# Kernel tuning notes

Hardware: AMD Instinct MI355X
Metric: run time of the kernel (lower is better)

Reference implementation:

```python
import jax, jax.numpy as jnp
import numpy as np

B, N_CGS, N_ATOMS, KNN, K, DEPTH = 16, 256, 1024, 32, 128, 3
CUTOFF = 10.0


def _init_params(key):
    ks = jax.random.split(key, 12)
    s = 1.0 / np.sqrt(K)
    p = {}
    # stacked per-depth settransform weights: Linear stored as [in, out] (y = x @ W + b)
    p['mlp_W1'] = jax.random.normal(ks[0], (DEPTH, K, K), jnp.float32) * s
    p['mlp_b1'] = jnp.zeros((DEPTH, K), jnp.float32)
    p['mlp_W2'] = jax.random.normal(ks[1], (DEPTH, K, K), jnp.float32) * s
    p['mlp_b2'] = jnp.zeros((DEPTH, K), jnp.float32)
    p['upd_W1'] = jax.random.normal(ks[2], (DEPTH, K, K), jnp.float32) * s
    p['upd_b1'] = jnp.zeros((DEPTH, K), jnp.float32)
    p['upd_W2'] = jax.random.normal(ks[3], (DEPTH, K, K), jnp.float32) * s
    p['upd_b2'] = jnp.zeros((DEPTH, K), jnp.float32)
    p['dec_W1'] = jax.random.normal(ks[4], (K, K), jnp.float32) * s
    p['dec_b1'] = jnp.zeros((K,), jnp.float32)
    p['dec_W2'] = jax.random.normal(ks[5], (K, N_ATOMS), jnp.float32) * s
    p['dec_b2'] = jnp.zeros((N_ATOMS,), jnp.float32)
    return p


def setup_inputs() -> dict:
    key = jax.random.key(0)
    ks = jax.random.split(key, 6)
    inp = {
        'soft_assign': jax.random.uniform(ks[0], (B, N_ATOMS, N_CGS), jnp.float32),
        'xyz': jax.random.normal(ks[1], (B, N_ATOMS, 3), jnp.float32),
        'cg_xyz': jax.random.normal(ks[2], (B, N_CGS, 3), jnp.float32),
        'assign_norm': jax.random.uniform(ks[3], (B, N_ATOMS, N_CGS), jnp.float32),
        'assign_idx': jax.random.randint(ks[4], (N_ATOMS,), 0, N_CGS, jnp.int32),
    }
    inp.update(_init_params(ks[5]))
    return inp


def _forward(cg_xyz, assign_norm, assign_idx,
             mlp_W1, mlp_b1, mlp_W2, mlp_b2,
             upd_W1, upd_b1, upd_W2, upd_b2,
             dec_W1, dec_b1, dec_W2, dec_b2):
    act = jax.nn.relu
    # Pairwise CG distance + ascending sort (as in source). The source then
    # zeroes sorted values beyond rank knn and uses value.nonzero()[:, 1:] as
    # neighbor pairs, i.e. it indexes by SORT RANK (ranks 1..knn), not by the
    # sorted index tensor knbrs. For generic (distinct) coordinates this is
    # exactly: neighbor j in {1..knn} for every center i. We replicate that.
    dist_vec = cg_xyz[:, None, 1:KNN + 1, :] - cg_xyz[:, :, None, :]  # [B, n_cgs, knn, 3]
    dist_vec = dist_vec.reshape(B, N_CGS * KNN, 3)
    dist = jnp.sqrt(jnp.sum(dist_vec ** 2, axis=-1)).reshape(B, N_CGS, KNN, 1)

    # GaussianSmearing(0, cutoff, feature_dim)
    offset = jnp.linspace(0.0, CUTOFF, K)  # [K]
    coeff = -0.5 / (offset[1] - offset[0]) ** 2
    out = jnp.exp(coeff * (dist - offset) ** 2)  # [B, n_cgs, knn, K]

    # settransform layers (loop over small fixed depth)
    for d in range(DEPTH):
        upd = act(out @ mlp_W1[d] + mlp_b1[d]) @ mlp_W2[d] + mlp_b2[d]
        cg_contract = jnp.mean(upd, axis=-2, keepdims=True)  # mean over knn axis
        h = upd + cg_contract
        out = act(h @ upd_W1[d] + upd_b1[d]) @ upd_W2[d] + upd_b2[d]

    # decode K -> n_atoms
    coeffs = (act(out @ dec_W1 + dec_b1) @ dec_W2 + dec_b2)
    coeffs = coeffs.reshape(B, N_CGS * KNN, N_ATOMS)

    dx_recon = jnp.einsum('bio,bin->bon', coeffs, dist_vec)      # [B, n_atoms, 3]
    cg_offset = jnp.einsum('bin,bij->bjn', dx_recon, assign_norm)  # [B, n_cgs, 3]
    cg_offset_lift = cg_offset[:, assign_idx, :]                  # [B, n_atoms, 3]
    xyz_recon = cg_xyz[:, assign_idx, :] - cg_offset_lift + dx_recon
    return xyz_recon


def reference(soft_assign, xyz, cg_xyz, assign_norm, assign_idx,
              mlp_W1, mlp_b1, mlp_W2, mlp_b2,
              upd_W1, upd_b1, upd_W2, upd_b2,
              dec_W1, dec_b1, dec_W2, dec_b2):
    xyz_recon = _forward(cg_xyz, assign_norm, assign_idx,
                         mlp_W1, mlp_b1, mlp_W2, mlp_b2,
                         upd_W1, upd_b1, upd_W2, upd_b2,
                         dec_W1, dec_b1, dec_W2, dec_b2)
    return (soft_assign, xyz, xyz_recon)
```

## Files before the change

kernel.cpp:

```cpp
#include <hip/hip_runtime.h>

#define BATCH   16
#define NCGS    256
#define NATOMS  1024
#define KNN     32
#define KF      128

typedef __attribute__((ext_vector_type(8))) short bf16x8;
typedef __attribute__((ext_vector_type(4))) float f32x4;

#define NFRAG (13*8*4)

__global__ __launch_bounds__(256)
void prep_kernel(const float* __restrict__ mlp_W1, const float* __restrict__ mlp_W2,
                 const float* __restrict__ upd_W1, const float* __restrict__ upd_W2,
                 const float* __restrict__ dec_W1, uint* __restrict__ Wswz)
{
    int t = blockIdx.x * 256 + threadIdx.x;
    if (t >= 13*8*4*64) return;
    int lane = t & 63;
    int kc   = (t >> 6) & 3;
    int ft   = (t >> 8) & 7;
    int s    = t >> 11;

    const float* W;
    if (s < 12) {
        int d = s >> 2, ph = s & 3;
        if      (ph == 0) W = mlp_W1 + d*KF*KF;
        else if (ph == 1) W = mlp_W2 + d*KF*KF;
        else if (ph == 2) W = upd_W1 + d*KF*KF;
        else              W = upd_W2 + d*KF*KF;
    } else W = dec_W1;

    int f  = ft*16 + (lane & 15);
    int kb = kc*32 + (lane >> 4)*8;

    uint hi[4], lo[4];
    #pragma unroll
    for (int w = 0; w < 4; ++w) {
        float v0 = W[(kb + 2*w    )*KF + f];
        float v1 = W[(kb + 2*w + 1)*KF + f];
        uint b0 = __float_as_uint(v0), b1 = __float_as_uint(v1);
        hi[w] = (b0 >> 16) | (b1 & 0xffff0000u);
        float l0 = v0 - __uint_as_float(b0 & 0xffff0000u);
        float l1 = v1 - __uint_as_float(b1 & 0xffff0000u);
        lo[w] = (__float_as_uint(l0) >> 16) | (__float_as_uint(l1) & 0xffff0000u);
    }
    int fi = (s*8 + ft)*4 + kc;
    uint* ph_ = Wswz + (size_t)((fi*2 + 0)*64 + lane)*4;
    uint* pl_ = Wswz + (size_t)((fi*2 + 1)*64 + lane)*4;
    #pragma unroll
    for (int w = 0; w < 4; ++w) { ph_[w] = hi[w]; pl_[w] = lo[w]; }
}

__global__ __launch_bounds__(256, 2)
void mlp_kernel(const float* __restrict__ cg_xyz, const bf16x8* __restrict__ Wf,
                const float* __restrict__ mlp_b1, const float* __restrict__ mlp_b2,
                const float* __restrict__ upd_b1, const float* __restrict__ upd_b2,
                const float* __restrict__ dec_b1, float* __restrict__ G)
{
    __shared__ __align__(16) short Fs[2][KF*KF];
    __shared__ float dvec[128*3];

    const int tid = threadIdx.x;
    const int wv  = tid >> 6;
    const int l   = tid & 63;
    const int b   = blockIdx.x >> 6;
    const int cg0 = (blockIdx.x & 63) * 4;
    const int cg  = cg0 + wv;

    char* hB = (char*)&Fs[0][0];
    char* lB = (char*)&Fs[1][0];

    const float* cgb = cg_xyz + (size_t)b * NCGS * 3;
    const int rl = l & 31;
    const int nb = 1 + rl;
    float dxv = cgb[nb*3+0] - cgb[cg*3+0];
    float dyv = cgb[nb*3+1] - cgb[cg*3+1];
    float dzv = cgb[nb*3+2] - cgb[cg*3+2];
    float dist = sqrtf(dxv*dxv + dyv*dyv + dzv*dzv);
    if (l < 32) {
        int r = wv*32 + rl;
        dvec[r*3+0] = dxv; dvec[r*3+1] = dyv; dvec[r*3+2] = dzv;
    }

    {
        const float STEP  = 10.0f / 127.0f;
        const float COEFF = -0.5f / (STEP * STEP);
        int r  = wv*32 + rl;
        int kh = (l >> 5) * 64;
        uint rb = (uint)r * 256;
        uint sw = (uint)(r & 7) << 4;
        #pragma unroll 8
        for (int j = 0; j < 32; ++j) {
            int k = kh + 2*j;
            float t0 = dist - (float)k * STEP;
            float t1 = dist - (float)(k+1) * STEP;
            float e0 = expf(COEFF * t0 * t0);
            float e1 = expf(COEFF * t1 * t1);
            uint b0 = __float_as_uint(e0), b1 = __float_as_uint(e1);
            uint hw = (b0 >> 16) | (b1 & 0xffff0000u);
            float l0 = e0 - __uint_as_float(b0 & 0xffff0000u);
            float l1 = e1 - __uint_as_float(b1 & 0xffff0000u);
            uint lw = (__float_as_uint(l0) >> 16) | (__float_as_uint(l1) & 0xffff0000u);
            uint off = rb + (((uint)(2*k)) ^ sw);
            *(uint*)(hB + off) = hw;
            *(uint*)(lB + off) = lw;
        }
    }

    for (int s = 0; s < 13; ++s) {
        const float* bias; int md;
        if (s < 12) {
            int d = s >> 2, ph = s & 3;
            if      (ph == 0) { bias = mlp_b1 + d*KF; md = 0; }
            else if (ph == 1) { bias = mlp_b2 + d*KF; md = 1; }
            else if (ph == 2) { bias = upd_b1 + d*KF; md = 0; }
            else              { bias = upd_b2 + d*KF; md = 2; }
        } else { bias = dec_b1; md = 0; }

        bf16x8 bf[2][4][2];
        #pragma unroll
        for (int rt = 0; rt < 2; ++rt) {
            int r = wv*32 + rt*16 + (l & 15);
            uint rb = (uint)r * 256;
            uint sw = (uint)(r & 7) << 4;
            #pragma unroll
            for (int kc = 0; kc < 4; ++kc) {
                uint cb = (uint)(kc*64 + ((l >> 4) << 4));
                uint off = rb + (cb ^ sw);
                bf[rt][kc][0] = *(const bf16x8*)(hB + off);
                bf[rt][kc][1] = *(const bf16x8*)(lB + off);
            }
        }

        f32x4 acc[8][2];
        #pragma unroll
        for (int ft = 0; ft < 8; ++ft)
            #pragma unroll
            for (int rt = 0; rt < 2; ++rt)
                acc[ft][rt] = (f32x4){0.f, 0.f, 0.f, 0.f};

        #pragma unroll
        for (int kc = 0; kc < 4; ++kc) {
            #pragma unroll
            for (int ft = 0; ft < 8; ++ft) {
                int fi = (s*8 + ft)*4 + kc;
                bf16x8 whi = Wf[(fi*2 + 0)*64 + l];
                bf16x8 wlo = Wf[(fi*2 + 1)*64 + l];
                #pragma unroll
                for (int rt = 0; rt < 2; ++rt) {
                    acc[ft][rt] = __builtin_amdgcn_mfma_f32_16x16x32_bf16(whi, bf[rt][kc][0], acc[ft][rt], 0, 0, 0);
                    acc[ft][rt] = __builtin_amdgcn_mfma_f32_16x16x32_bf16(whi, bf[rt][kc][1], acc[ft][rt], 0, 0, 0);
                    acc[ft][rt] = __builtin_amdgcn_mfma_f32_16x16x32_bf16(wlo, bf[rt][kc][0], acc[ft][rt], 0, 0, 0);
                }
            }
        }

        #pragma unroll
        for (int ft = 0; ft < 8; ++ft) {
            float4 bv = *(const float4*)(bias + ft*16 + ((l >> 4) << 2));
            #pragma unroll
            for (int rt = 0; rt < 2; ++rt) {
                acc[ft][rt][0] += bv.x; acc[ft][rt][1] += bv.y;
                acc[ft][rt][2] += bv.z; acc[ft][rt][3] += bv.w;
            }
        }
        if (md == 0) {
            #pragma unroll
            for (int ft = 0; ft < 8; ++ft)
                #pragma unroll
                for (int rt = 0; rt < 2; ++rt)
                    #pragma unroll
                    for (int q = 0; q < 4; ++q)
                        acc[ft][rt][q] = fmaxf(acc[ft][rt][q], 0.f);
        } else if (md == 1) {
            #pragma unroll
            for (int ft = 0; ft < 8; ++ft)
                #pragma unroll
                for (int q = 0; q < 4; ++q) {
                    float sm = acc[ft][0][q] + acc[ft][1][q];
                    sm += __shfl_xor(sm, 1);
                    sm += __shfl_xor(sm, 2);
                    sm += __shfl_xor(sm, 4);
                    sm += __shfl_xor(sm, 8);
                    float mn = sm * (1.0f / 32.0f);
                    acc[ft][0][q] += mn;
                    acc[ft][1][q] += mn;
                }
        }
        #pragma unroll
        for (int ft = 0; ft < 8; ++ft) {
            #pragma unroll
            for (int rt = 0; rt < 2; ++rt) {
                int r = wv*32 + rt*16 + (l & 15);
                uint sw  = (uint)(r & 7) << 4;
                uint off = (uint)r*256 + (((uint)(ft*32 + ((l >> 4) << 3))) ^ sw);
                uint b0 = __float_as_uint(acc[ft][rt][0]);
                uint b1 = __float_as_uint(acc[ft][rt][1]);
                uint b2 = __float_as_uint(acc[ft][rt][2]);
                uint b3 = __float_as_uint(acc[ft][rt][3]);
                uint2 hw, lw;
                hw.x = (b0 >> 16) | (b1 & 0xffff0000u);
                hw.y = (b2 >> 16) | (b3 & 0xffff0000u);
                float l0 = acc[ft][rt][0] - __uint_as_float(b0 & 0xffff0000u);
                float l1 = acc[ft][rt][1] - __uint_as_float(b1 & 0xffff0000u);
                float l2 = acc[ft][rt][2] - __uint_as_float(b2 & 0xffff0000u);
                float l3 = acc[ft][rt][3] - __uint_as_float(b3 & 0xffff0000u);
                lw.x = (__float_as_uint(l0) >> 16) | (__float_as_uint(l1) & 0xffff0000u);
                lw.y = (__float_as_uint(l2) >> 16) | (__float_as_uint(l3) & 0xffff0000u);
                *(uint2*)(hB + off) = hw;
                *(uint2*)(lB + off) = lw;
            }
        }
    }
    __syncthreads();

    {
        int k  = tid & 127;
        int rh = tid >> 7;
        float g0 = 0.f, g1 = 0.f, g2 = 0.f;
        #pragma unroll 4
        for (int rr = 0; rr < 64; ++rr) {
            int r = rh*64 + rr;
            uint off = (uint)r*256 + (((uint)(2*k)) ^ ((uint)(r & 7) << 4));
            uint hv = *(unsigned short*)(hB + off);
            uint lv = *(unsigned short*)(lB + off);
            float v = __uint_as_float(hv << 16) + __uint_as_float(lv << 16);
            g0 = fmaf(v, dvec[r*3+0], g0);
            g1 = fmaf(v, dvec[r*3+1], g1);
            g2 = fmaf(v, dvec[r*3+2], g2);
        }
        float* Gb = G + ((size_t)b * KF + k) * 3;
        atomicAdd(Gb+0, g0); atomicAdd(Gb+1, g1); atomicAdd(Gb+2, g2);
    }
}

__global__ __launch_bounds__(256)
void dx_kernel(const float* __restrict__ cg_xyz, const float* __restrict__ dec_W2,
               const float* __restrict__ dec_b2, const float* __restrict__ G,
               float* __restrict__ dxr)
{
    __shared__ float Gl[KF * 3];
    __shared__ float red[256 * 3];
    const int tid = threadIdx.x;
    const int b   = blockIdx.x >> 2;
    const int og  = blockIdx.x & 3;

    if (tid < 192) {
        Gl[tid]       = G[(size_t)b*KF*3 + tid];
        Gl[tid + 192] = G[(size_t)b*KF*3 + tid + 192];
    }
    const float* cgb = cg_xyz + (size_t)b * NCGS * 3;
    float w = ((tid >= 1 && tid <= 32) ? 256.f : 0.f) - 32.f;
    red[tid]       = w * cgb[tid*3+0];
    red[256 + tid] = w * cgb[tid*3+1];
    red[512 + tid] = w * cgb[tid*3+2];
    __syncthreads();
    for (int s2 = 128; s2 > 0; s2 >>= 1) {
        if (tid < s2) {
            red[tid]       += red[tid + s2];
            red[256 + tid] += red[256 + tid + s2];
            red[512 + tid] += red[512 + tid + s2];
        }
        __syncthreads();
    }
    const float S0 = red[0], S1 = red[256], S2 = red[512];

    const int o = og * 256 + tid;
    const float bq = dec_b2[o];
    float a0 = bq * S0, a1 = bq * S1, a2 = bq * S2;
    #pragma unroll 4
    for (int k = 0; k < KF; ++k) {
        float wvv = dec_W2[k * NATOMS + o];
        a0 = fmaf(wvv, Gl[k*3+0], a0);
        a1 = fmaf(wvv, Gl[k*3+1], a1);
        a2 = fmaf(wvv, Gl[k*3+2], a2);
    }
    float* dp = dxr + ((size_t)b * NATOMS + o) * 3;
    dp[0] = a0; dp[1] = a1; dp[2] = a2;
}

__global__ __launch_bounds__(256)
void cgo_kernel(const float* __restrict__ assign_norm, const float* __restrict__ dxr,
                float* __restrict__ cgo)
{
    __shared__ float dxl[64 * 3];
    const int tid = threadIdx.x;
    const int b   = blockIdx.x >> 4;
    const int a0  = (blockIdx.x & 15) * 64;
    if (tid < 192) dxl[tid] = dxr[((size_t)b * NATOMS + a0) * 3 + tid];
    __syncthreads();
    float c0 = 0.f, c1 = 0.f, c2 = 0.f;
    const float* an = assign_norm + ((size_t)b * NATOMS + a0) * NCGS + tid;
    #pragma unroll 4
    for (int a = 0; a < 64; ++a) {
        float v = an[(size_t)a * NCGS];
        c0 = fmaf(v, dxl[a*3+0], c0);
        c1 = fmaf(v, dxl[a*3+1], c1);
        c2 = fmaf(v, dxl[a*3+2], c2);
    }
    float* cp = cgo + ((size_t)b * NCGS + tid) * 3;
    atomicAdd(cp+0, c0); atomicAdd(cp+1, c1); atomicAdd(cp+2, c2);
}

__global__ __launch_bounds__(256)
void recon_kernel(const float* __restrict__ cg_xyz, const float* __restrict__ cgo,
                  const float* __restrict__ dxr, const int* __restrict__ assign_idx,
                  float* __restrict__ out)
{
    int i = blockIdx.x * 256 + threadIdx.x;
    int b   = i / (NATOMS * 3);
    int rem = i - b * (NATOMS * 3);
    int a   = rem / 3;
    int n   = rem - a * 3;
    int ia  = assign_idx[a];
    float v = cg_xyz[((size_t)b*NCGS + ia)*3 + n]
            - cgo[((size_t)b*NCGS + ia)*3 + n]
            + dxr[((size_t)b*NATOMS + a)*3 + n];
    out[i] = v;
}

extern "C" void kernel_launch(void* const* d_in, const int* in_sizes, int n_in,
                              void* d_out, int out_size, void* d_ws, size_t ws_size,
                              hipStream_t stream)
{
    const float* soft_assign = (const float*)d_in[0];
    const float* xyz         = (const float*)d_in[1];
    const float* cg_xyz      = (const float*)d_in[2];
    const float* assign_norm = (const float*)d_in[3];
    const int*   assign_idx  = (const int*)  d_in[4];
    const float* mlp_W1 = (const float*)d_in[5];
    const float* mlp_b1 = (const float*)d_in[6];
    const float* mlp_W2 = (const float*)d_in[7];
    const float* mlp_b2 = (const float*)d_in[8];
    const float* upd_W1 = (const float*)d_in[9];
    const float* upd_b1 = (const float*)d_in[10];
    const float* upd_W2 = (const float*)d_in[11];
    const float* upd_b2 = (const float*)d_in[12];
    const float* dec_W1 = (const float*)d_in[13];
    const float* dec_b1 = (const float*)d_in[14];
    const float* dec_W2 = (const float*)d_in[15];
    const float* dec_b2 = (const float*)d_in[16];

    float* out = (float*)d_out;

    uint*  Wswz = (uint*)d_ws;
    float* G    = (float*)d_ws + NFRAG*2*64*4;
    float* cgo  = G + BATCH * KF * 3;
    float* dxr  = cgo + BATCH * NCGS * 3;

    hipMemcpyAsync(out, soft_assign, (size_t)BATCH*NATOMS*NCGS*sizeof(float),
                   hipMemcpyDeviceToDevice, stream);
    hipMemcpyAsync(out + (size_t)BATCH*NATOMS*NCGS, xyz,
                   (size_t)BATCH*NATOMS*3*sizeof(float),
                   hipMemcpyDeviceToDevice, stream);
    hipMemsetAsync(G, 0, (size_t)(BATCH*KF*3 + BATCH*NCGS*3)*sizeof(float), stream);

    prep_kernel<<<104, 256, 0, stream>>>(mlp_W1, mlp_W2, upd_W1, upd_W2, dec_W1, Wswz);
    mlp_kernel<<<BATCH*64, 256, 0, stream>>>(cg_xyz, (const bf16x8*)Wswz,
        mlp_b1, mlp_b2, upd_b1, upd_b2, dec_b1, G);
    dx_kernel<<<BATCH*4, 256, 0, stream>>>(cg_xyz, dec_W2, dec_b2, G, dxr);
    cgo_kernel<<<BATCH*16, 256, 0, stream>>>(assign_norm, dxr, cgo);
    recon_kernel<<<(BATCH*NATOMS*3)/256, 256, 0, stream>>>(
        cg_xyz, cgo, dxr, assign_idx,
        out + (size_t)BATCH*NATOMS*NCGS + (size_t)BATCH*NATOMS*3);
}
```

Measured before the change: 341.7 us.

## Keep MLP activations in registers and permute weight K-order to skip LDS

The 13-stage MLP chain now keeps the hi/lo bf16 activation fragments in registers between stages instead of round-tripping them through shared memory. The weight prep permutes the K ordering for stages after the first so that MFMA accumulator outputs map directly onto the next stage's B-operand layout. The final G reduction is done with lane shuffles and scattered over 8 partial slices to spread atomic contention, and dx_kernel sums those slices. This removes LDS traffic and barriers and may raise occupancy, at the cost of higher register pressure and more atomics per block.

```diff
diff --git a/kernel.cpp b/kernel.cpp
--- a/kernel.cpp
+++ b/kernel.cpp
@@ -5,11 +5,14 @@
 #define NATOMS  1024
 #define KNN     32
 #define KF      128
+#define NSLICE  8
 
 typedef __attribute__((ext_vector_type(8))) short bf16x8;
 typedef __attribute__((ext_vector_type(4))) float f32x4;
 
 #define NFRAG (13*8*4)
+
+union U16B { bf16x8 v; uint u[4]; };
 
 __global__ __launch_bounds__(256)
 void prep_kernel(const float* __restrict__ mlp_W1, const float* __restrict__ mlp_W2,
@@ -32,14 +35,17 @@
         else              W = upd_W2 + d*KF*KF;
     } else W = dec_W1;
 
-    int f  = ft*16 + (lane & 15);
-    int kb = kc*32 + (lane >> 4)*8;
+    int f = ft*16 + (lane & 15);
+    int g = lane >> 4;
 
     uint hi[4], lo[4];
     #pragma unroll
     for (int w = 0; w < 4; ++w) {
-        float v0 = W[(kb + 2*w    )*KF + f];
-        float v1 = W[(kb + 2*w + 1)*KF + f];
+        int k0;
+        if (s == 0) k0 = kc*32 + g*8 + 2*w;
+        else        k0 = kc*16 + (w>>1)*64 + g*4 + 2*(w&1);
+        float v0 = W[(size_t)k0*KF + f];
+        float v1 = W[(size_t)(k0+1)*KF + f];
         uint b0 = __float_as_uint(v0), b1 = __float_as_uint(v1);
         hi[w] = (b0 >> 16) | (b1 & 0xffff0000u);
         float l0 = v0 - __uint_as_float(b0 & 0xffff0000u);
@@ -57,58 +63,50 @@
 void mlp_kernel(const float* __restrict__ cg_xyz, const bf16x8* __restrict__ Wf,
                 const float* __restrict__ mlp_b1, const float* __restrict__ mlp_b2,
                 const float* __restrict__ upd_b1, const float* __restrict__ upd_b2,
-                const float* __restrict__ dec_b1, float* __restrict__ G)
-{
-    __shared__ __align__(16) short Fs[2][KF*KF];
-    __shared__ float dvec[128*3];
-
+                const float* __restrict__ dec_b1, float* __restrict__ Gp)
+{
     const int tid = threadIdx.x;
     const int wv  = tid >> 6;
     const int l   = tid & 63;
+    const int g   = l >> 4;
+    const int e0  = l & 15;
     const int b   = blockIdx.x >> 6;
-    const int cg0 = (blockIdx.x & 63) * 4;
-    const int cg  = cg0 + wv;
-
-    char* hB = (char*)&Fs[0][0];
-    char* lB = (char*)&Fs[1][0];
+    const int cg  = (blockIdx.x & 63) * 4 + wv;
 
     const float* cgb = cg_xyz + (size_t)b * NCGS * 3;
-    const int rl = l & 31;
-    const int nb = 1 + rl;
-    float dxv = cgb[nb*3+0] - cgb[cg*3+0];
-    float dyv = cgb[nb*3+1] - cgb[cg*3+1];
-    float dzv = cgb[nb*3+2] - cgb[cg*3+2];
-    float dist = sqrtf(dxv*dxv + dyv*dyv + dzv*dzv);
-    if (l < 32) {
-        int r = wv*32 + rl;
-        dvec[r*3+0] = dxv; dvec[r*3+1] = dyv; dvec[r*3+2] = dzv;
-    }
-
-    {
-        const float STEP  = 10.0f / 127.0f;
-        const float COEFF = -0.5f / (STEP * STEP);
-        int r  = wv*32 + rl;
-        int kh = (l >> 5) * 64;
-        uint rb = (uint)r * 256;
-        uint sw = (uint)(r & 7) << 4;
-        #pragma unroll 8
-        for (int j = 0; j < 32; ++j) {
-            int k = kh + 2*j;
-            float t0 = dist - (float)k * STEP;
-            float t1 = dist - (float)(k+1) * STEP;
-            float e0 = expf(COEFF * t0 * t0);
-            float e1 = expf(COEFF * t1 * t1);
-            uint b0 = __float_as_uint(e0), b1 = __float_as_uint(e1);
-            uint hw = (b0 >> 16) | (b1 & 0xffff0000u);
-            float l0 = e0 - __uint_as_float(b0 & 0xffff0000u);
-            float l1 = e1 - __uint_as_float(b1 & 0xffff0000u);
-            uint lw = (__float_as_uint(l0) >> 16) | (__float_as_uint(l1) & 0xffff0000u);
-            uint off = rb + (((uint)(2*k)) ^ sw);
-            *(uint*)(hB + off) = hw;
-            *(uint*)(lB + off) = lw;
-        }
-    }
-
+    const float cx = cgb[cg*3+0], cy = cgb[cg*3+1], cz = cgb[cg*3+2];
+    const float d0x = cgb[(1+e0)*3+0]-cx,  d0y = cgb[(1+e0)*3+1]-cy,  d0z = cgb[(1+e0)*3+2]-cz;
+    const float d1x = cgb[(17+e0)*3+0]-cx, d1y = cgb[(17+e0)*3+1]-cy, d1z = cgb[(17+e0)*3+2]-cz;
+    const float dist0 = sqrtf(d0x*d0x + d0y*d0y + d0z*d0z);
+    const float dist1 = sqrtf(d1x*d1x + d1y*d1y + d1z*d1z);
+
+    const float STEP  = 10.0f / 127.0f;
+    const float COEFF = -0.5f / (STEP * STEP);
+    bf16x8 bh[2][4], bl[2][4];
+    #pragma unroll
+    for (int rt = 0; rt < 2; ++rt) {
+        float dd = rt ? dist1 : dist0;
+        #pragma unroll
+        for (int kc = 0; kc < 4; ++kc) {
+            U16B H, L;
+            #pragma unroll
+            for (int w = 0; w < 4; ++w) {
+                int k0 = kc*32 + g*8 + 2*w;
+                float t0 = dd - (float)k0 * STEP;
+                float t1 = dd - (float)(k0+1) * STEP;
+                float e0f = expf(COEFF * t0 * t0);
+                float e1f = expf(COEFF * t1 * t1);
+                uint b0 = __float_as_uint(e0f), b1 = __float_as_uint(e1f);
+                H.u[w] = (b0 >> 16) | (b1 & 0xffff0000u);
+                float l0 = e0f - __uint_as_float(b0 & 0xffff0000u);
+                float l1 = e1f - __uint_as_float(b1 & 0xffff0000u);
+                L.u[w] = (__float_as_uint(l0) >> 16) | (__float_as_uint(l1) & 0xffff0000u);
+            }
+            bh[rt][kc] = H.v; bl[rt][kc] = L.v;
+        }
+    }
+
+    f32x4 acc[8][2];
     for (int s = 0; s < 13; ++s) {
         const float* bias; int md;
         if (s < 12) {
@@ -119,22 +117,6 @@
             else              { bias = upd_b2 + d*KF; md = 2; }
         } else { bias = dec_b1; md = 0; }
 
-        bf16x8 bf[2][4][2];
-        #pragma unroll
-        for (int rt = 0; rt < 2; ++rt) {
-            int r = wv*32 + rt*16 + (l & 15);
-            uint rb = (uint)r * 256;
-            uint sw = (uint)(r & 7) << 4;
-            #pragma unroll
-            for (int kc = 0; kc < 4; ++kc) {
-                uint cb = (uint)(kc*64 + ((l >> 4) << 4));
-                uint off = rb + (cb ^ sw);
-                bf[rt][kc][0] = *(const bf16x8*)(hB + off);
-                bf[rt][kc][1] = *(const bf16x8*)(lB + off);
-            }
-        }
-
-        f32x4 acc[8][2];
         #pragma unroll
         for (int ft = 0; ft < 8; ++ft)
             #pragma unroll
@@ -150,16 +132,16 @@
                 bf16x8 wlo = Wf[(fi*2 + 1)*64 + l];
                 #pragma unroll
                 for (int rt = 0; rt < 2; ++rt) {
-                    acc[ft][rt] = __builtin_amdgcn_mfma_f32_16x16x32_bf16(whi, bf[rt][kc][0], acc[ft][rt], 0, 0, 0);
-                    acc[ft][rt] = __builtin_amdgcn_mfma_f32_16x16x32_bf16(whi, bf[rt][kc][1], acc[ft][rt], 0, 0, 0);
-                    acc[ft][rt] = __builtin_amdgcn_mfma_f32_16x16x32_bf16(wlo, bf[rt][kc][0], acc[ft][rt], 0, 0, 0);
+                    acc[ft][rt] = __builtin_amdgcn_mfma_f32_16x16x32_bf16(whi, bh[rt][kc], acc[ft][rt], 0, 0, 0);
+                    acc[ft][rt] = __builtin_amdgcn_mfma_f32_16x16x32_bf16(whi, bl[rt][kc], acc[ft][rt], 0, 0, 0);
+                    acc[ft][rt] = __builtin_amdgcn_mfma_f32_16x16x32_bf16(wlo, bh[rt][kc], acc[ft][rt], 0, 0, 0);
                 }
             }
         }
 
         #pragma unroll
         for (int ft = 0; ft < 8; ++ft) {
-            float4 bv = *(const float4*)(bias + ft*16 + ((l >> 4) << 2));
+            float4 bv = *(const float4*)(bias + ft*16 + g*4);
             #pragma unroll
             for (int rt = 0; rt < 2; ++rt) {
                 acc[ft][rt][0] += bv.x; acc[ft][rt][1] += bv.y;
@@ -189,56 +171,63 @@
                     acc[ft][1][q] += mn;
                 }
         }
-        #pragma unroll
-        for (int ft = 0; ft < 8; ++ft) {
-            #pragma unroll
-            for (int rt = 0; rt < 2; ++rt) {
-                int r = wv*32 + rt*16 + (l & 15);
-                uint sw  = (uint)(r & 7) << 4;
-                uint off = (uint)r*256 + (((uint)(ft*32 + ((l >> 4) << 3))) ^ sw);
-                uint b0 = __float_as_uint(acc[ft][rt][0]);
-                uint b1 = __float_as_uint(acc[ft][rt][1]);
-                uint b2 = __float_as_uint(acc[ft][rt][2]);
-                uint b3 = __float_as_uint(acc[ft][rt][3]);
-                uint2 hw, lw;
-                hw.x = (b0 >> 16) | (b1 & 0xffff0000u);
-                hw.y = (b2 >> 16) | (b3 & 0xffff0000u);
-                float l0 = acc[ft][rt][0] - __uint_as_float(b0 & 0xffff0000u);
-                float l1 = acc[ft][rt][1] - __uint_as_float(b1 & 0xffff0000u);
-                float l2 = acc[ft][rt][2] - __uint_as_float(b2 & 0xffff0000u);
-                float l3 = acc[ft][rt][3] - __uint_as_float(b3 & 0xffff0000u);
-                lw.x = (__float_as_uint(l0) >> 16) | (__float_as_uint(l1) & 0xffff0000u);
-                lw.y = (__float_as_uint(l2) >> 16) | (__float_as_uint(l3) & 0xffff0000u);
-                *(uint2*)(hB + off) = hw;
-                *(uint2*)(lB + off) = lw;
+
+        if (s < 12) {
+            #pragma unroll
+            for (int rt = 0; rt < 2; ++rt)
+                #pragma unroll
+                for (int kc = 0; kc < 4; ++kc) {
+                    float v0 = acc[kc  ][rt][0], v1 = acc[kc  ][rt][1];
+                    float v2 = acc[kc  ][rt][2], v3 = acc[kc  ][rt][3];
+                    float v4 = acc[kc+4][rt][0], v5 = acc[kc+4][rt][1];
+                    float v6 = acc[kc+4][rt][2], v7 = acc[kc+4][rt][3];
+                    uint u0=__float_as_uint(v0), u1=__float_as_uint(v1);
+                    uint u2=__float_as_uint(v2), u3=__float_as_uint(v3);
+                    uint u4=__float_as_uint(v4), u5=__float_as_uint(v5);
+                    uint u6=__float_as_uint(v6), u7=__float_as_uint(v7);
+                    U16B H, L;
+                    H.u[0] = (u0>>16)|(u1&0xffff0000u);
+                    H.u[1] = (u2>>16)|(u3&0xffff0000u);
+                    H.u[2] = (u4>>16)|(u5&0xffff0000u);
+                    H.u[3] = (u6>>16)|(u7&0xffff0000u);
+                    float l0=v0-__uint_as_float(u0&0xffff0000u), l1=v1-__uint_as_float(u1&0xffff0000u);
+                    float l2=v2-__uint_as_float(u2&0xffff0000u), l3=v3-__uint_as_float(u3&0xffff0000u);
+                    float l4=v4-__uint_as_float(u4&0xffff0000u), l5=v5-__uint_as_float(u5&0xffff0000u);
+                    float l6=v6-__uint_as_float(u6&0xffff0000u), l7=v7-__uint_as_float(u7&0xffff0000u);
+                    L.u[0] = (__float_as_uint(l0)>>16)|(__float_as_uint(l1)&0xffff0000u);
+                    L.u[1] = (__float_as_uint(l2)>>16)|(__float_as_uint(l3)&0xffff0000u);
+                    L.u[2] = (__float_as_uint(l4)>>16)|(__float_as_uint(l5)&0xffff0000u);
+                    L.u[3] = (__float_as_uint(l6)>>16)|(__float_as_uint(l7)&0xffff0000u);
+                    bh[rt][kc] = H.v; bl[rt][kc] = L.v;
+                }
+        }
+    }
+
+    const int slice = blockIdx.x & (NSLICE-1);
+    float* Gb = Gp + ((size_t)slice*BATCH + b) * KF * 3;
+    #pragma unroll
+    for (int ft = 0; ft < 8; ++ft) {
+        #pragma unroll
+        for (int q = 0; q < 4; ++q) {
+            float r0 = acc[ft][0][q], r1 = acc[ft][1][q];
+            float px = r0*d0x + r1*d1x;
+            float py = r0*d0y + r1*d1y;
+            float pz = r0*d0z + r1*d1z;
+            px += __shfl_xor(px, 1); py += __shfl_xor(py, 1); pz += __shfl_xor(pz, 1);
+            px += __shfl_xor(px, 2); py += __shfl_xor(py, 2); pz += __shfl_xor(pz, 2);
+            px += __shfl_xor(px, 4); py += __shfl_xor(py, 4); pz += __shfl_xor(pz, 4);
+            px += __shfl_xor(px, 8); py += __shfl_xor(py, 8); pz += __shfl_xor(pz, 8);
+            if (e0 < 3) {
+                float pv = (e0 == 0) ? px : ((e0 == 1) ? py : pz);
+                atomicAdd(Gb + (16*ft + 4*g + q)*3 + e0, pv);
             }
         }
-    }
-    __syncthreads();
-
-    {
-        int k  = tid & 127;
-        int rh = tid >> 7;
-        float g0 = 0.f, g1 = 0.f, g2 = 0.f;
-        #pragma unroll 4
-        for (int rr = 0; rr < 64; ++rr) {
-            int r = rh*64 + rr;
-            uint off = (uint)r*256 + (((uint)(2*k)) ^ ((uint)(r & 7) << 4));
-            uint hv = *(unsigned short*)(hB + off);
-            uint lv = *(unsigned short*)(lB + off);
-            float v = __uint_as_float(hv << 16) + __uint_as_float(lv << 16);
-            g0 = fmaf(v, dvec[r*3+0], g0);
-            g1 = fmaf(v, dvec[r*3+1], g1);
-            g2 = fmaf(v, dvec[r*3+2], g2);
-        }
-        float* Gb = G + ((size_t)b * KF + k) * 3;
-        atomicAdd(Gb+0, g0); atomicAdd(Gb+1, g1); atomicAdd(Gb+2, g2);
     }
 }
 
 __global__ __launch_bounds__(256)
 void dx_kernel(const float* __restrict__ cg_xyz, const float* __restrict__ dec_W2,
-               const float* __restrict__ dec_b2, const float* __restrict__ G,
+               const float* __restrict__ dec_b2, const float* __restrict__ Gp,
                float* __restrict__ dxr)
 {
     __shared__ float Gl[KF * 3];
@@ -248,8 +237,13 @@
     const int og  = blockIdx.x & 3;
 
     if (tid < 192) {
-        Gl[tid]       = G[(size_t)b*KF*3 + tid];
-        Gl[tid + 192] = G[(size_t)b*KF*3 + tid + 192];
+        float s0 = 0.f, s1 = 0.f;
+        #pragma unroll
+        for (int sl = 0; sl < NSLICE; ++sl) {
+            const float* gp = Gp + ((size_t)sl*BATCH + b) * KF * 3;
+            s0 += gp[tid]; s1 += gp[tid + 192];
+        }
+        Gl[tid] = s0; Gl[tid + 192] = s1;
     }
     const float* cgb = cg_xyz + (size_t)b * NCGS * 3;
     float w = ((tid >= 1 && tid <= 32) ? 256.f : 0.f) - 32.f;
@@ -346,8 +340,8 @@
     float* out = (float*)d_out;
 
     uint*  Wswz = (uint*)d_ws;
-    float* G    = (float*)d_ws + NFRAG*2*64*4;
-    float* cgo  = G + BATCH * KF * 3;
+    float* Gp   = (float*)d_ws + NFRAG*2*64*4;
+    float* cgo  = Gp + NSLICE * BATCH * KF * 3;
     float* dxr  = cgo + BATCH * NCGS * 3;
 
     hipMemcpyAsync(out, soft_assign, (size_t)BATCH*NATOMS*NCGS*sizeof(float),
@@ -355,12 +349,13 @@
     hipMemcpyAsync(out + (size_t)BATCH*NATOMS*NCGS, xyz,
                    (size_t)BATCH*NATOMS*3*sizeof(float),
                    hipMemcpyDeviceToDevice, stream);
-    hipMemsetAsync(G, 0, (size_t)(BATCH*KF*3 + BATCH*NCGS*3)*sizeof(float), stream);
+    hipMemsetAsync(Gp, 0,
+        (size_t)(NSLICE*BATCH*KF*3 + BATCH*NCGS*3)*sizeof(float), stream);
 
     prep_kernel<<<104, 256, 0, stream>>>(mlp_W1, mlp_W2, upd_W1, upd_W2, dec_W1, Wswz);
     mlp_kernel<<<BATCH*64, 256, 0, stream>>>(cg_xyz, (const bf16x8*)Wswz,
-        mlp_b1, mlp_b2, upd_b1, upd_b2, dec_b1, G);
-    dx_kernel<<<BATCH*4, 256, 0, stream>>>(cg_xyz, dec_W2, dec_b2, G, dxr);
+        mlp_b1, mlp_b2, upd_b1, upd_b2, dec_b1, Gp);
+    dx_kernel<<<BATCH*4, 256, 0, stream>>>(cg_xyz, dec_W2, dec_b2, Gp, dxr);
     cgo_kernel<<<BATCH*16, 256, 0, stream>>>(assign_norm, dxr, cgo);
     recon_kernel<<<(BATCH*NATOMS*3)/256, 256, 0, stream>>>(
         cg_xyz, cgo, dxr, assign_idx,
```

Measured after the change: 362.9 us. 6.2% more time.
